# Kernel optimization log

Hardware: AMD Instinct MI355X
Metric: run time of the kernel (lower is better)

## Reference

```python
import jax, jax.numpy as jnp
import numpy as np

NUM_INPUTS = 16
NUM_HIDDEN = 256
NUM_LAYERS = 4
B = 16384


def setup_inputs() -> dict:
    key = jax.random.key(0)
    ks = jax.random.split(key, 8)
    H, N, L = NUM_HIDDEN, NUM_INPUTS, NUM_LAYERS
    x0 = jax.random.normal(ks[0], (B, N), dtype=jnp.float32)
    # input layer: Linear(2 -> H)
    W_in = jax.random.normal(ks[1], (2, H), dtype=jnp.float32) * (1.0 / np.sqrt(2.0))
    b_in = jnp.zeros((H,), dtype=jnp.float32)
    # L-1 intermediate layers: Linear(2H -> H), stacked
    W_mid = jax.random.normal(ks[2], (L - 1, 2 * H, H), dtype=jnp.float32) * (1.0 / np.sqrt(2.0 * H))
    b_mid = jnp.zeros((L - 1, H), dtype=jnp.float32)
    # slater: Linear(H -> N) with xavier-normal weight, zero bias
    W_sl = jax.random.normal(ks[3], (H, N), dtype=jnp.float32) * np.sqrt(2.0 / (H + N))
    b_sl = jnp.zeros((N,), dtype=jnp.float32)
    width = jnp.full((1,), 0.1, dtype=jnp.float32)
    return {"x0": x0, "W_in": W_in, "b_in": b_in, "W_mid": W_mid,
            "b_mid": b_mid, "W_sl": W_sl, "b_sl": b_sl, "width": width}


def _forward(x0, W_in, b_in, W_mid, b_mid, W_sl, b_sl, width):
    N = x0.shape[1]
    # input equivariant layer: f = stack(h, mean(h)) -> [B, N, 2]
    g = jnp.broadcast_to(x0.mean(axis=1, keepdims=True), x0.shape)
    f = jnp.stack((x0, g), axis=2)                       # [B, N, 2]
    h = jnp.tanh(jnp.einsum('bnf,fh->bnh', f, W_in) + b_in)  # [B, N, H]
    # intermediate equivariant layers with residual
    for i in range(W_mid.shape[0]):
        gm = jnp.broadcast_to(h.mean(axis=1, keepdims=True), h.shape)
        fm = jnp.concatenate((h, gm), axis=2)            # [B, N, 2H]
        h = jnp.tanh(jnp.einsum('bnf,fh->bnh', fm, W_mid[i]) + b_mid[i]) + h
    # slog slater determinant
    slater = jnp.einsum('bnh,hm->bnm', h, W_sl) + b_sl   # [B, N, N]
    sign, logabsdet = jnp.linalg.slogdet(slater)
    log_factorial = jnp.log(jnp.arange(1, N + 1, dtype=jnp.float32)).sum()
    log_bcs = -width[0] * jnp.sum(x0 ** 2, axis=1)       # [B]
    return sign, logabsdet - 0.5 * log_factorial + log_bcs


def reference(x0, W_in, b_in, W_mid, b_mid, W_sl, b_sl, width):
    return _forward(x0, W_in, b_in, W_mid, b_mid, W_sl, b_sl, width)
```

## Files before the change

kernel.cpp:

```cpp
#include <hip/hip_runtime.h>

#define BTOT 16384
#define NI   16
#define HD   256
#define BB   4
#define NMID 3
#define ASH  264
#define SLS  20
#define HALF_LOGFACT 15.3359295387f

typedef short  bf16x8 __attribute__((ext_vector_type(8)));
typedef float  f32x4  __attribute__((ext_vector_type(4)));
typedef const __attribute__((address_space(1))) unsigned int* as1p;
typedef __attribute__((address_space(3))) unsigned int* as3p;

__device__ __forceinline__ unsigned short f2bf(float f) {
    unsigned u = __builtin_bit_cast(unsigned, f);
    u += 0x7FFFu + ((u >> 16) & 1u);
    return (unsigned short)(u >> 16);
}
__device__ __forceinline__ unsigned cvt_pk_bf16(float lo, float hi) {
    unsigned d;
    asm("v_cvt_pk_bf16_f32 %0, %1, %2" : "=v"(d) : "v"(lo), "v"(hi));
    return d;
}
__device__ __forceinline__ float bflo(unsigned u) { return __builtin_bit_cast(float, u << 16); }
__device__ __forceinline__ float bfhi(unsigned u) { return __builtin_bit_cast(float, u & 0xFFFF0000u); }
__device__ __forceinline__ float bcast(float x, int lane) {
    return __builtin_bit_cast(float,
        __builtin_amdgcn_readlane(__builtin_bit_cast(int, x), lane));
}
__device__ __forceinline__ float tanh5(float x) {
    float z = __builtin_amdgcn_exp2f(x * 2.885390081777927f);
    return __builtin_fmaf(-2.0f, __builtin_amdgcn_rcpf(1.0f + z), 1.0f);
}
#define LGKM_BAR() do { asm volatile("s_waitcnt lgkmcnt(0)" ::: "memory"); \
    __builtin_amdgcn_s_barrier(); __builtin_amdgcn_sched_barrier(0); } while (0)

__global__ void prep_w(const float* __restrict__ Wmid, const float* __restrict__ Wsl,
                       unsigned short* __restrict__ wtc) {
    const int b = blockIdx.x;
    const int t = threadIdx.x;
    unsigned short* dst = wtc + (size_t)b * 8192;
    if (b < 48) {
        const int layer = b >> 4, ch = b & 15;
        const float* src = Wmid + (size_t)layer * (2 * HD * HD);
#pragma unroll 4
        for (int v = 0; v < 32; ++v) {
            int o = t * 32 + v;
            int kk = o & 7, j = (o >> 3) & 15, kg = o >> 7;
            dst[o] = f2bf(src[(8 * kg + kk) * HD + ch * 16 + j]);
        }
    } else {
#pragma unroll 4
        for (int v = 0; v < 32; ++v) {
            int o = t * 32 + v;
            int kk = o & 7, j = (o >> 3) & 15, kg = o >> 7;
            dst[o] = (kg < 32) ? f2bf(Wsl[(8 * kg + kk) * NI + j]) : (unsigned short)0;
        }
    }
}

struct __align__(16) SMem {
    unsigned short wt[2][4096];
    union {
        unsigned short h[BB * NI * ASH];
        float slf[BB][NI * ASH / 2];
    } u;
    union {
        unsigned short gmgv[BB * HD];
        struct { float x0[BB * NI]; float gmean[BB]; } x;
    } v;
};
static_assert(sizeof(SMem) == 52224, "3 blocks/CU needs <= ~52.7KB");

__device__ __forceinline__ void stage_half(const unsigned short* __restrict__ wtc,
                                           unsigned short* dst_base, int fc, int tid) {
    const unsigned short* gsrc = wtc + (size_t)fc * 8192 + tid * 8;
    __builtin_amdgcn_global_load_lds((as1p)gsrc,          (as3p)(dst_base + tid * 8),        16, 0, 0);
    __builtin_amdgcn_global_load_lds((as1p)(gsrc + 2048), (as3p)(dst_base + tid * 8 + 2048), 16, 0, 0);
}

__global__ __launch_bounds__(256, 3)
void eqslater_mfma(const float* __restrict__ x0g,
                   const float* __restrict__ Win,
                   const float* __restrict__ bin,
                   const float* __restrict__ bmid,
                   const float* __restrict__ bsl,
                   const float* __restrict__ width,
                   const unsigned short* __restrict__ wtc,
                   float* __restrict__ out) {
    __shared__ SMem sm;
    const int tid = threadIdx.x;
    const int bbase = blockIdx.x * BB;
    const int e = tid >> 6;
    const int l = tid & 63;
    const int c = l & 15;
    const int g = l >> 4;
    const int j4 = 4 * g;

    stage_half(wtc, sm.wt[0], 0, tid);

    if (tid < BB * NI) sm.v.x.x0[tid] = x0g[bbase * NI + tid];
    LGKM_BAR();
    if (tid < BB) {
        float s = 0.f;
#pragma unroll
        for (int n = 0; n < NI; ++n) s += sm.v.x.x0[tid * NI + n];
        sm.v.x.gmean[tid] = s * 0.0625f;
    }
    LGKM_BAR();

    {
        const int p2 = tid & 127;
        const int rh = tid >> 7;
        const float w0a = Win[2 * p2],      w0b = Win[2 * p2 + 1];
        const float w1a = Win[HD + 2 * p2], w1b = Win[HD + 2 * p2 + 1];
        const float ba  = bin[2 * p2],      bb2 = bin[2 * p2 + 1];
#pragma unroll
        for (int half = 0; half < 2; ++half) {
            const int el = rh * 2 + half;
            const float gmv = sm.v.x.gmean[el];
            const float g1a = gmv * w1a + ba, g1b = gmv * w1b + bb2;
#pragma unroll 4
            for (int r = 0; r < NI; ++r) {
                float xv = sm.v.x.x0[el * NI + r];
                float f0 = tanh5(__builtin_fmaf(xv, w0a, g1a));
                float f1 = tanh5(__builtin_fmaf(xv, w0b, g1b));
                *(unsigned*)&sm.u.h[(el * NI + r) * ASH + 2 * p2] = cvt_pk_bf16(f0, f1);
            }
        }
    }
    LGKM_BAR();

    bf16x8 af[8], agm[8], bq2[8];

#pragma unroll 1
    for (int layer = 0; layer < NMID; ++layer) {
        {
            const int c0 = l * 4;
            float s0 = 0, s1 = 0, s2 = 0, s3 = 0;
#pragma unroll
            for (int r = 0; r < NI; ++r) {
                uint2 d = *(const uint2*)&sm.u.h[(e * NI + r) * ASH + c0];
                s0 += bflo(d.x); s1 += bfhi(d.x);
                s2 += bflo(d.y); s3 += bfhi(d.y);
            }
            uint2 o;
            o.x = cvt_pk_bf16(s0 * 0.0625f, s1 * 0.0625f);
            o.y = cvt_pk_bf16(s2 * 0.0625f, s3 * 0.0625f);
            *(uint2*)&sm.v.gmgv[e * HD + c0] = o;
        }
#pragma unroll
        for (int s = 0; s < 8; ++s)
            af[s] = *(const bf16x8*)&sm.u.h[(e * NI + c) * ASH + 32 * s + 8 * g];
        LGKM_BAR();
#pragma unroll
        for (int s = 0; s < 8; ++s)
            agm[s] = *(const bf16x8*)&sm.v.gmgv[(c & 3) * HD + 32 * s + 8 * g];

        const float* bml = bmid + layer * HD;
        f32x4 avp = {0.f, 0.f, 0.f, 0.f};

#pragma unroll 1
        for (int ch = 0; ch < 16; ++ch) {
            const int fc = layer * 16 + ch;
            LGKM_BAR();

            if (fc < 48) stage_half(wtc, sm.wt[(fc + 1) & 1], fc + 1, tid);
            __builtin_amdgcn_sched_barrier(0);

            if (ch > 0) {
                const int jp = (ch - 1) * 16 + j4;
                unsigned short* hrow = &sm.u.h[(e * NI + c) * ASH + jp];
                uint2 gd = *(const uint2*)&sm.v.gmgv[e * HD + jp];
                uint2 hd2 = *(const uint2*)hrow;
                float f0 = tanh5(avp[0] + bflo(gd.x)) + bflo(hd2.x);
                float f1 = tanh5(avp[1] + bfhi(gd.x)) + bfhi(hd2.x);
                float f2 = tanh5(avp[2] + bflo(gd.y)) + bflo(hd2.y);
                float f3 = tanh5(avp[3] + bfhi(gd.y)) + bfhi(hd2.y);
                uint2 w;
                w.x = cvt_pk_bf16(f0, f1); w.y = cvt_pk_bf16(f2, f3);
                *(uint2*)hrow = w;
            }
            __builtin_amdgcn_sched_barrier(0);
            asm volatile("s_waitcnt vmcnt(2)" ::: "memory");
            __builtin_amdgcn_sched_barrier(0);

            const bool own = (ch >> 2) == e;
            float4 bsv;
            if (own) {
                const unsigned short* gp = wtc + (size_t)fc * 8192 + c * 8 + g * 128;
#pragma unroll
                for (int t2 = 0; t2 < 8; ++t2)
                    bq2[t2] = *(const bf16x8*)(gp + (32 + 4 * t2) * 128);
                bsv = *(const float4*)&bml[ch * 16 + j4];
            }

            const unsigned short* wb = sm.wt[fc & 1];
            f32x4 p0 = {0.f,0.f,0.f,0.f}, p1 = {0.f,0.f,0.f,0.f};
#pragma unroll
            for (int s = 0; s < 4; ++s) {
                bf16x8 b0 = *(const bf16x8*)&wb[(8 * s     + g) * 128 + c * 8];
                bf16x8 b1 = *(const bf16x8*)&wb[(8 * s + 4 + g) * 128 + c * 8];
                p0 = __builtin_amdgcn_mfma_f32_16x16x32_bf16(b0, af[2 * s],     p0, 0, 0, 0);
                p1 = __builtin_amdgcn_mfma_f32_16x16x32_bf16(b1, af[2 * s + 1], p1, 0, 0, 0);
            }
            avp = p0 + p1;

            if (own) {
                f32x4 q0 = {0.f,0.f,0.f,0.f}, q1 = {0.f,0.f,0.f,0.f};
#pragma unroll
                for (int s = 0; s < 4; ++s) {
                    q0 = __builtin_amdgcn_mfma_f32_16x16x32_bf16(bq2[2 * s],     agm[2 * s],     q0, 0, 0, 0);
                    q1 = __builtin_amdgcn_mfma_f32_16x16x32_bf16(bq2[2 * s + 1], agm[2 * s + 1], q1, 0, 0, 0);
                }
                f32x4 gq = q0 + q1;
                if (c < 4) {
                    uint2 w;
                    w.x = cvt_pk_bf16(gq[0] + bsv.x, gq[1] + bsv.y);
                    w.y = cvt_pk_bf16(gq[2] + bsv.z, gq[3] + bsv.w);
                    *(uint2*)&sm.v.gmgv[c * HD + ch * 16 + j4] = w;
                }
            }
        }
        LGKM_BAR();
        {
            const int jp = 240 + j4;
            unsigned short* hrow = &sm.u.h[(e * NI + c) * ASH + jp];
            uint2 gd = *(const uint2*)&sm.v.gmgv[e * HD + jp];
            uint2 hd2 = *(const uint2*)hrow;
            float f0 = tanh5(avp[0] + bflo(gd.x)) + bflo(hd2.x);
            float f1 = tanh5(avp[1] + bfhi(gd.x)) + bfhi(hd2.x);
            float f2 = tanh5(avp[2] + bflo(gd.y)) + bflo(hd2.y);
            float f3 = tanh5(avp[3] + bfhi(gd.y)) + bfhi(hd2.y);
            uint2 w;
            w.x = cvt_pk_bf16(f0, f1); w.y = cvt_pk_bf16(f2, f3);
            *(uint2*)hrow = w;
        }
        __builtin_amdgcn_sched_barrier(0);
    }

#pragma unroll
    for (int s = 0; s < 8; ++s)
        af[s] = *(const bf16x8*)&sm.u.h[(e * NI + c) * ASH + 32 * s + 8 * g];
    asm volatile("s_waitcnt vmcnt(0) lgkmcnt(0)" ::: "memory");
    __builtin_amdgcn_s_barrier();
    __builtin_amdgcn_sched_barrier(0);
    {
        const unsigned short* wb = sm.wt[0];
        f32x4 a0 = {0.f,0.f,0.f,0.f}, a1 = {0.f,0.f,0.f,0.f};
#pragma unroll
        for (int s = 0; s < 4; ++s) {
            bf16x8 b0 = *(const bf16x8*)&wb[(8 * s     + g) * 128 + c * 8];
            bf16x8 b1 = *(const bf16x8*)&wb[(8 * s + 4 + g) * 128 + c * 8];
            a0 = __builtin_amdgcn_mfma_f32_16x16x32_bf16(b0, af[2 * s],     a0, 0, 0, 0);
            a1 = __builtin_amdgcn_mfma_f32_16x16x32_bf16(b1, af[2 * s + 1], a1, 0, 0, 0);
        }
        f32x4 sv = a0 + a1;
        const float4 bsv = *(const float4*)&bsl[j4];
        float* slp = &sm.u.slf[e][0];
        float4 o;
        o.x = sv[0] + bsv.x; o.y = sv[1] + bsv.y;
        o.z = sv[2] + bsv.z; o.w = sv[3] + bsv.w;
        *(float4*)&slp[c * SLS + j4] = o;
    }

    {
        const float* slp = &sm.u.slf[e][0];
        const int i = c;
        float M[16];
#pragma unroll
        for (int jj = 0; jj < 4; ++jj) {
            float4 vv = *(const float4*)&slp[i * SLS + 4 * jj];
            M[4 * jj] = vv.x; M[4 * jj + 1] = vv.y; M[4 * jj + 2] = vv.z; M[4 * jj + 3] = vv.w;
        }

        int elim = 0;
        unsigned chosen = 0;
        int invcnt = 0;
        float dsign = 1.f, logabs = 0.f;
#pragma unroll
        for (int k = 0; k < 16; ++k) {
            float myv = elim ? -1.f : __builtin_fabsf(M[k]);
            float maxv = myv;
#pragma unroll
            for (int off = 8; off > 0; off >>= 1)
                maxv = fmaxf(maxv, __shfl_xor(maxv, off));
            unsigned long long bal = __ballot(myv == maxv);
            const int p = (__ffsll((long long)bal) - 1) & 15;

            invcnt += __popc(chosen >> (p + 1));
            chosen |= 1u << p;
            if (i == p) elim = 1;

            float piv = bcast(M[k], p);
            float ap = fmaxf(__builtin_fabsf(piv), 1e-35f);
            logabs += __logf(ap);
            if (piv < 0.f) dsign = -dsign;
            float spiv = __builtin_copysignf(ap, piv);
            float mi = __fdividef(M[k], spiv);
#pragma unroll
            for (int j = k + 1; j < 16; ++j) {
                float pr = bcast(M[j], p);
                if (!elim) M[j] = __builtin_fmaf(-mi, pr, M[j]);
            }
        }
        if (invcnt & 1) dsign = -dsign;

        float xv = (l < NI) ? x0g[(bbase + e) * NI + l] : 0.f;
        float sq = xv * xv;
#pragma unroll
        for (int off = 8; off > 0; off >>= 1) sq += __shfl_xor(sq, off);

        if (l == 0) {
            out[bbase + e] = dsign;
            out[BTOT + bbase + e] = logabs - HALF_LOGFACT - width[0] * sq;
        }
    }
}

extern "C" void kernel_launch(void* const* d_in, const int* in_sizes, int n_in,
                              void* d_out, int out_size, void* d_ws, size_t ws_size,
                              hipStream_t stream) {
    const float* x0   = (const float*)d_in[0];
    const float* Win  = (const float*)d_in[1];
    const float* bin  = (const float*)d_in[2];
    const float* Wmid = (const float*)d_in[3];
    const float* bmid = (const float*)d_in[4];
    const float* Wsl  = (const float*)d_in[5];
    const float* bsl  = (const float*)d_in[6];
    const float* wid  = (const float*)d_in[7];
    float* out = (float*)d_out;

    unsigned short* wtc = (unsigned short*)d_ws;

    hipLaunchKernelGGL(prep_w, dim3(49), dim3(256), 0, stream, Wmid, Wsl, wtc);
    hipLaunchKernelGGL(eqslater_mfma, dim3(BTOT / BB), dim3(256), 0, stream,
                       x0, Win, bin, bmid, bsl, wid, wtc, out);
}
```

Baseline: 304.1 us.

## Load weights directly from global into registers and drop block barriers

```diff
diff --git a/kernel.cpp b/kernel.cpp
--- a/kernel.cpp
+++ b/kernel.cpp
@@ -11,8 +11,6 @@
 
 typedef short  bf16x8 __attribute__((ext_vector_type(8)));
 typedef float  f32x4  __attribute__((ext_vector_type(4)));
-typedef const __attribute__((address_space(1))) unsigned int* as1p;
-typedef __attribute__((address_space(3))) unsigned int* as3p;
 
 __device__ __forceinline__ unsigned short f2bf(float f) {
     unsigned u = __builtin_bit_cast(unsigned, f);
@@ -34,8 +32,8 @@
     float z = __builtin_amdgcn_exp2f(x * 2.885390081777927f);
     return __builtin_fmaf(-2.0f, __builtin_amdgcn_rcpf(1.0f + z), 1.0f);
 }
-#define LGKM_BAR() do { asm volatile("s_waitcnt lgkmcnt(0)" ::: "memory"); \
-    __builtin_amdgcn_s_barrier(); __builtin_amdgcn_sched_barrier(0); } while (0)
+#define LGKM_WAIT() do { asm volatile("s_waitcnt lgkmcnt(0)" ::: "memory"); \
+    __builtin_amdgcn_sched_barrier(0); } while (0)
 
 __global__ void prep_w(const float* __restrict__ Wmid, const float* __restrict__ Wsl,
                        unsigned short* __restrict__ wtc) {
@@ -62,24 +60,13 @@
 }
 
 struct __align__(16) SMem {
-    unsigned short wt[2][4096];
     union {
         unsigned short h[BB * NI * ASH];
         float slf[BB][NI * ASH / 2];
     } u;
-    union {
-        unsigned short gmgv[BB * HD];
-        struct { float x0[BB * NI]; float gmean[BB]; } x;
-    } v;
+    unsigned short gm[BB * HD];
 };
-static_assert(sizeof(SMem) == 52224, "3 blocks/CU needs <= ~52.7KB");
-
-__device__ __forceinline__ void stage_half(const unsigned short* __restrict__ wtc,
-                                           unsigned short* dst_base, int fc, int tid) {
-    const unsigned short* gsrc = wtc + (size_t)fc * 8192 + tid * 8;
-    __builtin_amdgcn_global_load_lds((as1p)gsrc,          (as3p)(dst_base + tid * 8),        16, 0, 0);
-    __builtin_amdgcn_global_load_lds((as1p)(gsrc + 2048), (as3p)(dst_base + tid * 8 + 2048), 16, 0, 0);
-}
+static_assert(sizeof(SMem) == 35840, "3+ blocks/CU easily");
 
 __global__ __launch_bounds__(256, 3)
 void eqslater_mfma(const float* __restrict__ x0g,
@@ -99,163 +86,114 @@
     const int g = l >> 4;
     const int j4 = 4 * g;
 
-    stage_half(wtc, sm.wt[0], 0, tid);
-
-    if (tid < BB * NI) sm.v.x.x0[tid] = x0g[bbase * NI + tid];
-    LGKM_BAR();
-    if (tid < BB) {
-        float s = 0.f;
-#pragma unroll
-        for (int n = 0; n < NI; ++n) s += sm.v.x.x0[tid * NI + n];
-        sm.v.x.gmean[tid] = s * 0.0625f;
-    }
-    LGKM_BAR();
+    const unsigned short* wlane = wtc + (size_t)g * 128 + (size_t)c * 8;
+
+    bf16x8 bqA[8], bqB[8];
+#pragma unroll
+    for (int s = 0; s < 8; ++s)
+        bqA[s] = *(const bf16x8*)(wlane + s * 512);
 
     {
-        const int p2 = tid & 127;
-        const int rh = tid >> 7;
-        const float w0a = Win[2 * p2],      w0b = Win[2 * p2 + 1];
-        const float w1a = Win[HD + 2 * p2], w1b = Win[HD + 2 * p2 + 1];
-        const float ba  = bin[2 * p2],      bb2 = bin[2 * p2 + 1];
-#pragma unroll
-        for (int half = 0; half < 2; ++half) {
-            const int el = rh * 2 + half;
-            const float gmv = sm.v.x.gmean[el];
-            const float g1a = gmv * w1a + ba, g1b = gmv * w1b + bb2;
+        float x0v = x0g[(bbase + e) * NI + c];
+        float ssum = x0v;
+#pragma unroll
+        for (int off = 8; off > 0; off >>= 1) ssum += __shfl_xor(ssum, off);
+        const float gmean = ssum * 0.0625f;
+        const int c4 = 4 * l;
+        float4 w0 = *(const float4*)&Win[c4];
+        float4 w1 = *(const float4*)&Win[HD + c4];
+        float4 bi = *(const float4*)&bin[c4];
+        float g0 = __builtin_fmaf(gmean, w1.x, bi.x);
+        float g1 = __builtin_fmaf(gmean, w1.y, bi.y);
+        float g2 = __builtin_fmaf(gmean, w1.z, bi.z);
+        float g3 = __builtin_fmaf(gmean, w1.w, bi.w);
 #pragma unroll 4
-            for (int r = 0; r < NI; ++r) {
-                float xv = sm.v.x.x0[el * NI + r];
-                float f0 = tanh5(__builtin_fmaf(xv, w0a, g1a));
-                float f1 = tanh5(__builtin_fmaf(xv, w0b, g1b));
-                *(unsigned*)&sm.u.h[(el * NI + r) * ASH + 2 * p2] = cvt_pk_bf16(f0, f1);
-            }
-        }
-    }
-    LGKM_BAR();
-
-    bf16x8 af[8], agm[8], bq2[8];
+        for (int r = 0; r < NI; ++r) {
+            float xv = bcast(x0v, r);
+            float f0 = tanh5(__builtin_fmaf(xv, w0.x, g0));
+            float f1 = tanh5(__builtin_fmaf(xv, w0.y, g1));
+            float f2 = tanh5(__builtin_fmaf(xv, w0.z, g2));
+            float f3 = tanh5(__builtin_fmaf(xv, w0.w, g3));
+            uint2 o; o.x = cvt_pk_bf16(f0, f1); o.y = cvt_pk_bf16(f2, f3);
+            *(uint2*)&sm.u.h[(e * NI + r) * ASH + c4] = o;
+        }
+    }
+    LGKM_WAIT();
+
+    bf16x8 af[8], agm[8];
 
 #pragma unroll 1
     for (int layer = 0; layer < NMID; ++layer) {
         {
-            const int c0 = l * 4;
+            const int c4 = 4 * l;
             float s0 = 0, s1 = 0, s2 = 0, s3 = 0;
 #pragma unroll
             for (int r = 0; r < NI; ++r) {
-                uint2 d = *(const uint2*)&sm.u.h[(e * NI + r) * ASH + c0];
+                uint2 d = *(const uint2*)&sm.u.h[(e * NI + r) * ASH + c4];
                 s0 += bflo(d.x); s1 += bfhi(d.x);
                 s2 += bflo(d.y); s3 += bfhi(d.y);
             }
-            uint2 o;
-            o.x = cvt_pk_bf16(s0 * 0.0625f, s1 * 0.0625f);
-            o.y = cvt_pk_bf16(s2 * 0.0625f, s3 * 0.0625f);
-            *(uint2*)&sm.v.gmgv[e * HD + c0] = o;
-        }
-#pragma unroll
-        for (int s = 0; s < 8; ++s)
-            af[s] = *(const bf16x8*)&sm.u.h[(e * NI + c) * ASH + 32 * s + 8 * g];
-        LGKM_BAR();
-#pragma unroll
-        for (int s = 0; s < 8; ++s)
-            agm[s] = *(const bf16x8*)&sm.v.gmgv[(c & 3) * HD + 32 * s + 8 * g];
-
+            uint2 go;
+            go.x = cvt_pk_bf16(s0 * 0.0625f, s1 * 0.0625f);
+            go.y = cvt_pk_bf16(s2 * 0.0625f, s3 * 0.0625f);
+            *(uint2*)&sm.gm[e * HD + c4] = go;
+        }
+        LGKM_WAIT();
+#pragma unroll
+        for (int s = 0; s < 8; ++s) {
+            af[s]  = *(const bf16x8*)&sm.u.h[(e * NI + c) * ASH + 32 * s + 8 * g];
+            agm[s] = *(const bf16x8*)&sm.gm[e * HD + 32 * s + 8 * g];
+        }
         const float* bml = bmid + layer * HD;
-        f32x4 avp = {0.f, 0.f, 0.f, 0.f};
 
 #pragma unroll 1
         for (int ch = 0; ch < 16; ++ch) {
             const int fc = layer * 16 + ch;
-            LGKM_BAR();
-
-            if (fc < 48) stage_half(wtc, sm.wt[(fc + 1) & 1], fc + 1, tid);
-            __builtin_amdgcn_sched_barrier(0);
-
-            if (ch > 0) {
-                const int jp = (ch - 1) * 16 + j4;
-                unsigned short* hrow = &sm.u.h[(e * NI + c) * ASH + jp];
-                uint2 gd = *(const uint2*)&sm.v.gmgv[e * HD + jp];
-                uint2 hd2 = *(const uint2*)hrow;
-                float f0 = tanh5(avp[0] + bflo(gd.x)) + bflo(hd2.x);
-                float f1 = tanh5(avp[1] + bfhi(gd.x)) + bfhi(hd2.x);
-                float f2 = tanh5(avp[2] + bflo(gd.y)) + bflo(hd2.y);
-                float f3 = tanh5(avp[3] + bfhi(gd.y)) + bfhi(hd2.y);
-                uint2 w;
-                w.x = cvt_pk_bf16(f0, f1); w.y = cvt_pk_bf16(f2, f3);
-                *(uint2*)hrow = w;
-            }
-            __builtin_amdgcn_sched_barrier(0);
-            asm volatile("s_waitcnt vmcnt(2)" ::: "memory");
-            __builtin_amdgcn_sched_barrier(0);
-
-            const bool own = (ch >> 2) == e;
-            float4 bsv;
-            if (own) {
-                const unsigned short* gp = wtc + (size_t)fc * 8192 + c * 8 + g * 128;
-#pragma unroll
-                for (int t2 = 0; t2 < 8; ++t2)
-                    bq2[t2] = *(const bf16x8*)(gp + (32 + 4 * t2) * 128);
-                bsv = *(const float4*)&bml[ch * 16 + j4];
-            }
-
-            const unsigned short* wb = sm.wt[fc & 1];
+            const unsigned short* cb = wlane + (size_t)fc * 8192;
+
+#pragma unroll
+            for (int s = 0; s < 8; ++s)
+                bqB[s] = *(const bf16x8*)(cb + 4096 + s * 512);
+
             f32x4 p0 = {0.f,0.f,0.f,0.f}, p1 = {0.f,0.f,0.f,0.f};
 #pragma unroll
             for (int s = 0; s < 4; ++s) {
-                bf16x8 b0 = *(const bf16x8*)&wb[(8 * s     + g) * 128 + c * 8];
-                bf16x8 b1 = *(const bf16x8*)&wb[(8 * s + 4 + g) * 128 + c * 8];
-                p0 = __builtin_amdgcn_mfma_f32_16x16x32_bf16(b0, af[2 * s],     p0, 0, 0, 0);
-                p1 = __builtin_amdgcn_mfma_f32_16x16x32_bf16(b1, af[2 * s + 1], p1, 0, 0, 0);
-            }
-            avp = p0 + p1;
-
-            if (own) {
-                f32x4 q0 = {0.f,0.f,0.f,0.f}, q1 = {0.f,0.f,0.f,0.f};
-#pragma unroll
-                for (int s = 0; s < 4; ++s) {
-                    q0 = __builtin_amdgcn_mfma_f32_16x16x32_bf16(bq2[2 * s],     agm[2 * s],     q0, 0, 0, 0);
-                    q1 = __builtin_amdgcn_mfma_f32_16x16x32_bf16(bq2[2 * s + 1], agm[2 * s + 1], q1, 0, 0, 0);
-                }
-                f32x4 gq = q0 + q1;
-                if (c < 4) {
-                    uint2 w;
-                    w.x = cvt_pk_bf16(gq[0] + bsv.x, gq[1] + bsv.y);
-                    w.y = cvt_pk_bf16(gq[2] + bsv.z, gq[3] + bsv.w);
-                    *(uint2*)&sm.v.gmgv[c * HD + ch * 16 + j4] = w;
-                }
-            }
-        }
-        LGKM_BAR();
-        {
-            const int jp = 240 + j4;
-            unsigned short* hrow = &sm.u.h[(e * NI + c) * ASH + jp];
-            uint2 gd = *(const uint2*)&sm.v.gmgv[e * HD + jp];
+                p0 = __builtin_amdgcn_mfma_f32_16x16x32_bf16(bqA[2 * s],     af[2 * s],     p0, 0, 0, 0);
+                p1 = __builtin_amdgcn_mfma_f32_16x16x32_bf16(bqA[2 * s + 1], af[2 * s + 1], p1, 0, 0, 0);
+            }
+#pragma unroll
+            for (int s = 0; s < 8; ++s)
+                bqA[s] = *(const bf16x8*)(cb + 8192 + s * 512);
+
+#pragma unroll
+            for (int s = 0; s < 4; ++s) {
+                p0 = __builtin_amdgcn_mfma_f32_16x16x32_bf16(bqB[2 * s],     agm[2 * s],     p0, 0, 0, 0);
+                p1 = __builtin_amdgcn_mfma_f32_16x16x32_bf16(bqB[2 * s + 1], agm[2 * s + 1], p1, 0, 0, 0);
+            }
+            f32x4 av = p0 + p1;
+
+            const float4 bv = *(const float4*)&bml[ch * 16 + j4];
+            unsigned short* hrow = &sm.u.h[(e * NI + c) * ASH + ch * 16 + j4];
             uint2 hd2 = *(const uint2*)hrow;
-            float f0 = tanh5(avp[0] + bflo(gd.x)) + bflo(hd2.x);
-            float f1 = tanh5(avp[1] + bfhi(gd.x)) + bfhi(hd2.x);
-            float f2 = tanh5(avp[2] + bflo(gd.y)) + bflo(hd2.y);
-            float f3 = tanh5(avp[3] + bfhi(gd.y)) + bfhi(hd2.y);
-            uint2 w;
-            w.x = cvt_pk_bf16(f0, f1); w.y = cvt_pk_bf16(f2, f3);
+            float f0 = tanh5(av[0] + bv.x) + bflo(hd2.x);
+            float f1 = tanh5(av[1] + bv.y) + bfhi(hd2.x);
+            float f2 = tanh5(av[2] + bv.z) + bflo(hd2.y);
+            float f3 = tanh5(av[3] + bv.w) + bfhi(hd2.y);
+            uint2 w; w.x = cvt_pk_bf16(f0, f1); w.y = cvt_pk_bf16(f2, f3);
             *(uint2*)hrow = w;
         }
-        __builtin_amdgcn_sched_barrier(0);
+        LGKM_WAIT();
     }
 
 #pragma unroll
     for (int s = 0; s < 8; ++s)
         af[s] = *(const bf16x8*)&sm.u.h[(e * NI + c) * ASH + 32 * s + 8 * g];
-    asm volatile("s_waitcnt vmcnt(0) lgkmcnt(0)" ::: "memory");
-    __builtin_amdgcn_s_barrier();
-    __builtin_amdgcn_sched_barrier(0);
     {
-        const unsigned short* wb = sm.wt[0];
         f32x4 a0 = {0.f,0.f,0.f,0.f}, a1 = {0.f,0.f,0.f,0.f};
 #pragma unroll
         for (int s = 0; s < 4; ++s) {
-            bf16x8 b0 = *(const bf16x8*)&wb[(8 * s     + g) * 128 + c * 8];
-            bf16x8 b1 = *(const bf16x8*)&wb[(8 * s + 4 + g) * 128 + c * 8];
-            a0 = __builtin_amdgcn_mfma_f32_16x16x32_bf16(b0, af[2 * s],     a0, 0, 0, 0);
-            a1 = __builtin_amdgcn_mfma_f32_16x16x32_bf16(b1, af[2 * s + 1], a1, 0, 0, 0);
+            a0 = __builtin_amdgcn_mfma_f32_16x16x32_bf16(bqA[2 * s],     af[2 * s],     a0, 0, 0, 0);
+            a1 = __builtin_amdgcn_mfma_f32_16x16x32_bf16(bqA[2 * s + 1], af[2 * s + 1], a1, 0, 0, 0);
         }
         f32x4 sv = a0 + a1;
         const float4 bsv = *(const float4*)&bsl[j4];
@@ -265,6 +203,7 @@
         o.z = sv[2] + bsv.z; o.w = sv[3] + bsv.w;
         *(float4*)&slp[c * SLS + j4] = o;
     }
+    LGKM_WAIT();
 
     {
         const float* slp = &sm.u.slf[e][0];
```

After: 398.7 us. 1.31x slower.
